# Optimization experiments

Hardware: AMD Instinct MI355X
Metric: run time of the kernel (lower is better)

The kernel has to match this reference:

```python
import jax, jax.numpy as jnp
import numpy as np

N_ATOMS = 10000
N_PAIRS = 100000
H = 64          # hidden_channels
R = 32          # number_of_radial_basis_functions
MAX_Z = 100
CUTOFF = 0.5    # nm (radial_max_distance), min = 0.0


def cosine_cutoff(d):
    # 0.5*(cos(pi*d/rc)+1) for d < rc else 0
    return jnp.where(d < CUTOFF, 0.5 * (jnp.cos(jnp.pi * d / CUTOFF) + 1.0), 0.0)


def expnormal_rbf(d):
    # ExpNormal smearing (TorchMD/TensorNet style), cutoff_lower = 0
    start = float(np.exp(-CUTOFF))
    means = jnp.linspace(start, 1.0, R, dtype=d.dtype)            # [R]
    beta = (2.0 / R * (1.0 - start)) ** -2
    alpha = 5.0 / CUTOFF
    return jnp.exp(-beta * (jnp.exp(-alpha * d)[:, None] - means) ** 2)  # [P,R]


def vector_to_skewtensor(v):
    x, y, z = v[:, 0], v[:, 1], v[:, 2]
    o = jnp.zeros_like(x)
    return jnp.stack([o, -z, y, z, o, -x, -y, x, o], axis=-1).reshape(-1, 3, 3)


def vector_to_symtensor(v):
    t = v[:, :, None] * v[:, None, :]                              # [P,3,3]
    tr3 = (t[:, 0, 0] + t[:, 1, 1] + t[:, 2, 2]) / 3.0
    return t - tr3[:, None, None] * jnp.eye(3, dtype=v.dtype)


def setup_inputs() -> dict:
    key = jax.random.key(0)
    ks = jax.random.split(key, 20)
    atomic_numbers = jax.random.randint(ks[0], (N_ATOMS,), 0, MAX_Z)
    pair_indices = jax.random.randint(ks[1], (2, N_PAIRS), 0, N_ATOMS)
    r_ij = jax.random.normal(ks[2], (N_PAIRS, 3), dtype=jnp.float32) * 0.12  # ~0.2 nm norms
    d_ij = jnp.linalg.norm(r_ij, axis=-1, keepdims=True) + 1e-6
    s = 0.1
    p = {
        'emb':    jax.random.normal(ks[3], (MAX_Z, H)) * s,
        'emb2_w': jax.random.normal(ks[4], (H, 2 * H)) * s,
        'emb2_b': jnp.zeros((H,)),
        'dp1_w':  jax.random.normal(ks[5], (H, R)) * s,
        'dp1_b':  jnp.zeros((H,)),
        'dp2_w':  jax.random.normal(ks[6], (H, R)) * s,
        'dp2_b':  jnp.zeros((H,)),
        'dp3_w':  jax.random.normal(ks[7], (H, R)) * s,
        'dp3_b':  jnp.zeros((H,)),
        'lt0_w':  jax.random.normal(ks[8], (H, H)) * s,
        'lt1_w':  jax.random.normal(ks[9], (H, H)) * s,
        'lt2_w':  jax.random.normal(ks[10], (H, H)) * s,
        'ls1_w':  jax.random.normal(ks[11], (2 * H, H)) * s,
        'ls1_b':  jnp.zeros((2 * H,)),
        'ls2_w':  jax.random.normal(ks[12], (3 * H, 2 * H)) * s,
        'ls2_b':  jnp.zeros((3 * H,)),
        'ln_g':   jnp.ones((H,)),
        'ln_b':   jnp.zeros((H,)),
    }
    return dict(atomic_numbers=atomic_numbers, pair_indices=pair_indices,
                d_ij=d_ij, r_ij=r_ij, **p)


def reference(atomic_numbers, pair_indices, d_ij, r_ij,
              emb, emb2_w, emb2_b, dp1_w, dp1_b, dp2_w, dp2_b, dp3_w, dp3_b,
              lt0_w, lt1_w, lt2_w, ls1_w, ls1_b, ls2_w, ls2_b, ln_g, ln_b):
    n_atoms = atomic_numbers.shape[0]
    src = pair_indices[0]
    # atomic number message Zij: concat(emb[i], emb[j]) -> Linear
    zi = emb[atomic_numbers]                                      # [N,H]
    zij = jnp.concatenate([zi[src], zi[pair_indices[1]]], axis=-1)  # [P,2H]
    Zij = zij @ emb2_w.T + emb2_b                                 # [P,H]
    d = d_ij[:, 0]                                                # [P]
    unit = r_ij / d_ij                                            # [P,3]
    rc = cosine_cutoff(d)                                         # [P]
    rbf = expnormal_rbf(d) * rc[:, None]                          # [P,R]
    C = rc[:, None] * Zij                                         # [P,H]
    f1 = (rbf @ dp1_w.T + dp1_b) * C                              # [P,H]
    f2 = (rbf @ dp2_w.T + dp2_b) * C * 10.0                       # Angstrom scale
    f3 = (rbf @ dp3_w.T + dp3_b) * C * 100.0
    eye = jnp.eye(3, dtype=r_ij.dtype)
    skew = vector_to_skewtensor(unit)                             # [P,3,3]
    sym = vector_to_symtensor(unit)                               # [P,3,3]
    Iij = f1[:, :, None, None] * eye                              # [P,H,3,3]
    Aij = f2[:, :, None, None] * skew[:, None]
    Sij = f3[:, :, None, None] * sym[:, None]
    I = jax.ops.segment_sum(Iij, src, num_segments=n_atoms)       # [N,H,3,3]
    A = jax.ops.segment_sum(Aij, src, num_segments=n_atoms)
    S = jax.ops.segment_sum(Sij, src, num_segments=n_atoms)
    # tensor_norm -> LayerNorm -> scalar MLP
    tn = jnp.sum((I + A + S) ** 2, axis=(-2, -1))                 # [N,H]
    mu = tn.mean(-1, keepdims=True)
    var = tn.var(-1, keepdims=True)
    norm = (tn - mu) / jnp.sqrt(var + 1e-5) * ln_g + ln_b
    norm = jax.nn.silu(norm @ ls1_w.T + ls1_b)
    norm = jax.nn.silu(norm @ ls2_w.T + ls2_b)                    # [N,3H]
    norm = norm.reshape(-1, H, 3)
    I = jnp.einsum('nhij,gh->ngij', I, lt0_w) * norm[:, :, 0][:, :, None, None]
    A = jnp.einsum('nhij,gh->ngij', A, lt1_w) * norm[:, :, 1][:, :, None, None]
    S = jnp.einsum('nhij,gh->ngij', S, lt2_w) * norm[:, :, 2][:, :, None, None]
    return I + A + S
```

## Files before the change

### kernel.cpp

```cpp
#include <hip/hip_runtime.h>
#include <hip/hip_bf16.h>

#define N_ATOMS 10000
#define N_PAIRS 100000
#define HH 64
#define MAXZ 100

typedef _Float16 h2_t __attribute__((ext_vector_type(2)));

constexpr float RBF_START = 0.6065306597126334f;
constexpr float RBF_STEP  = (1.0f - RBF_START) / 31.0f;
constexpr float RBF_BETA  = 1.0f / ((0.0625f * (1.0f - RBF_START)) * (0.0625f * (1.0f - RBF_START)));
constexpr float LOG2E     = 1.4426950408889634f;
constexpr float NEG_ALPHA_L2 = -10.0f * LOG2E;
constexpr float NEG_BETA_L2  = -RBF_BETA * LOG2E;

#define OFF_EMB   0
#define OFF_W2    6400
#define OFF_B2    14592
#define OFF_D1W   14656
#define OFF_D1B   16704
#define OFF_D2W   16768
#define OFF_D2B   18816
#define OFF_D3W   18880
#define OFF_D3B   20928
#define OFF_LT0   20992
#define OFF_LT1   25088
#define OFF_LT2   29184
#define OFF_L1W   33280
#define OFF_L1B   41472
#define OFF_L2W   41600
#define OFF_L2B   66176
#define OFF_LNG   66368
#define OFF_LNB   66432
#define N_PARAMF  66496

#define PH_DP   0
#define PH_L1   3072
#define PH_L2   7168
#define PH_LT   19456
#define PH_N    25600

#define WS_WF     0
#define WS_CNT    266240
#define WS_OFF    307200
#define WS_CUR    348160
#define WS_T1     389120
#define WS_T2     414720
#define WS_PH     440320
#define WS_DPK    542720
#define WS_ZNL    2142720
#define WS_ACCH   2542720

__device__ __forceinline__ float bf2f(unsigned short u) {
    return __uint_as_float(((unsigned int)u) << 16);
}
__device__ __forceinline__ float fexp2(float x) { return __builtin_amdgcn_exp2f(x); }
__device__ __forceinline__ float fcos2pi(float x) { return __builtin_amdgcn_cosf(x); }
__device__ __forceinline__ float fsilu(float x) { return x / (1.0f + fexp2(-LOG2E * x)); }
__device__ __forceinline__ h2_t u2h(unsigned u) { return __builtin_bit_cast(h2_t, u); }
__device__ __forceinline__ unsigned packh2(float a, float b) {
    h2_t v; v.x = (_Float16)a; v.y = (_Float16)b;
    return __builtin_bit_cast(unsigned, v);
}

#if __has_builtin(__builtin_amdgcn_fdot2)
__device__ __forceinline__ float FDOT2(h2_t a, h2_t b, float c) {
    return __builtin_amdgcn_fdot2(a, b, c, false);
}
#else
__device__ __forceinline__ float FDOT2(h2_t a, h2_t b, float c) {
    return c + (float)a.x * (float)b.x + (float)a.y * (float)b.y;
}
#endif
__device__ __forceinline__ float dot16h(const uint4* w, const uint4* x, float acc) {
    uint4 a = *w, b = *x;
    acc = FDOT2(u2h(a.x), u2h(b.x), acc);
    acc = FDOT2(u2h(a.y), u2h(b.y), acc);
    acc = FDOT2(u2h(a.z), u2h(b.z), acc);
    acc = FDOT2(u2h(a.w), u2h(b.w), acc);
    return acc;
}
__device__ __forceinline__ float dot16v(uint4 a, uint4 b, float acc) {
    acc = FDOT2(u2h(a.x), u2h(b.x), acc);
    acc = FDOT2(u2h(a.y), u2h(b.y), acc);
    acc = FDOT2(u2h(a.z), u2h(b.z), acc);
    acc = FDOT2(u2h(a.w), u2h(b.w), acc);
    return acc;
}

__device__ int classify64(const unsigned short* b, int lane) {
    unsigned short x = b[lane];
    int e = (x >> 7) & 0xFF;
    bool implaus = (x != 0) && (e < 96 || e > 133);
    bool zeroeven = ((lane & 1) == 0) && (x == 0);
    unsigned long long mi = __ballot(implaus);
    unsigned long long mz = __ballot(zeroeven);
    if (__popcll(mz) == 32) return 0;
    if (__popcll(mi) >= 8) return 0;
    return 1;
}

struct ConvArgs { const void* src[18]; float* dst; };

__global__ void k_prep(ConvArgs a, const int* __restrict__ pidx, int* __restrict__ cnt) {
    const int sizes[18] = {6400,8192,64,2048,64,2048,64,2048,64,4096,4096,4096,8192,128,24576,192,64,64};
    __shared__ int fl;
    if (threadIdx.x < 64) {
        int f = classify64((const unsigned short*)a.src[0], threadIdx.x);
        if (threadIdx.x == 0) fl = f;
    }
    __syncthreads();
    int t = blockIdx.x * 256 + threadIdx.x;
    if (t < N_PARAMF) {
        int acc = 0, seg = 0, off = t;
        #pragma unroll
        for (int i = 0; i < 18; ++i) {
            if (t >= acc && t < acc + sizes[i]) { seg = i; off = t - acc; }
            acc += sizes[i];
        }
        if (fl == 1) a.dst[t] = bf2f(((const unsigned short*)a.src[seg])[off]);
        else         a.dst[t] = ((const float*)a.src[seg])[off];
    }
    if (t < N_PAIRS) atomicAdd(&cnt[pidx[t]], 1);
}

__global__ void k_tabpack(const float* __restrict__ WF, float* __restrict__ T1,
                          float* __restrict__ T2, unsigned* __restrict__ PH) {
    int z = blockIdx.x;
    int h = threadIdx.x;
    if (h < 64) {
        const float* ez = WF + OFF_EMB + z * HH;
        const float* w2 = WF + OFF_W2 + h * 128;
        float s1 = 0.f, s2 = 0.f;
        #pragma unroll
        for (int k = 0; k < 64; ++k) {
            float e = ez[k];
            s1 += w2[k] * e;
            s2 += w2[64 + k] * e;
        }
        T1[z * HH + h] = s1;
        T2[z * HH + h] = s2;
    }
    int q = blockIdx.x * 256 + threadIdx.x;
    int src;
    if (q < PH_L1) {
        int w = q >> 10, r = q & 1023;
        src = (w == 0 ? OFF_D1W : (w == 1 ? OFF_D2W : OFF_D3W)) + r * 2;
    } else if (q < PH_L2) {
        src = OFF_L1W + (q - PH_L1) * 2;
    } else if (q < PH_LT) {
        src = OFF_L2W + (q - PH_L2) * 2;
    } else {
        src = OFF_LT0 + (q - PH_LT) * 2;
    }
    PH[q] = packh2(WF[src], WF[src + 1]);
}

__global__ void k_scan(const int* __restrict__ cnt, int* __restrict__ offs, int* __restrict__ cur) {
    __shared__ int buf[1024];
    int tid = threadIdx.x;
    int base = tid * 10;
    int c[10]; int s = 0;
    #pragma unroll
    for (int i = 0; i < 10; ++i) {
        int idx = base + i;
        int v = (idx < N_ATOMS) ? cnt[idx] : 0;
        c[i] = v; s += v;
    }
    buf[tid] = s;
    __syncthreads();
    for (int off = 1; off < 1024; off <<= 1) {
        int v = (tid >= off) ? buf[tid - off] : 0;
        __syncthreads();
        buf[tid] += v;
        __syncthreads();
    }
    int run = buf[tid] - s;
    #pragma unroll
    for (int i = 0; i < 10; ++i) {
        int idx = base + i;
        if (idx < N_ATOMS) { offs[idx] = run; cur[idx] = run; run += c[i]; }
    }
    if (tid == 0) offs[N_ATOMS] = N_PAIRS;
}

__global__ void k_fill(const int* __restrict__ pidx, const int* __restrict__ an,
                       const void* __restrict__ dij_v, const void* __restrict__ rij_v,
                       int* __restrict__ cur,
                       float4* __restrict__ dpack, int* __restrict__ znl) {
    __shared__ int fdr[2];
    if (threadIdx.x < 64) {
        int fd = classify64((const unsigned short*)dij_v, threadIdx.x);
        int fr = classify64((const unsigned short*)rij_v, threadIdx.x);
        if (threadIdx.x == 0) { fdr[0] = fd; fdr[1] = fr; }
    }
    __syncthreads();
    int p = blockIdx.x * 256 + threadIdx.x;
    if (p >= N_PAIRS) return;
    int s = pidx[p];
    int dst = pidx[N_PAIRS + p];
    int pos = atomicAdd(&cur[s], 1);
    float d, rx, ry, rz;
    if (fdr[0] == 1) d = bf2f(((const unsigned short*)dij_v)[p]);
    else             d = ((const float*)dij_v)[p];
    if (fdr[1] == 1) {
        const unsigned short* r = (const unsigned short*)rij_v;
        rx = bf2f(r[3*p]); ry = bf2f(r[3*p+1]); rz = bf2f(r[3*p+2]);
    } else {
        const float* r = (const float*)rij_v;
        rx = r[3*p]; ry = r[3*p+1]; rz = r[3*p+2];
    }
    dpack[pos] = make_float4(rx, ry, rz, d);
    znl[pos] = an[dst];
}

__global__ __launch_bounds__(256, 4) void k_pair(
    const int* __restrict__ an,
    const float* __restrict__ WF,
    const int* __restrict__ offs,
    const float4* __restrict__ dpack, const int* __restrict__ znl,
    const float* __restrict__ T1, const float* __restrict__ T2,
    const unsigned* __restrict__ PH,
    unsigned* __restrict__ accH)
{
    __shared__ __align__(16) unsigned rbq[4 * 16];

    const int wave = threadIdx.x >> 6;
    const int h    = threadIdx.x & 63;
    const int n    = blockIdx.x * 4 + wave;

    _Float16* rbfh = (_Float16*)&rbq[wave * 16];
    const uint4* rbp = (const uint4*)&rbq[wave * 16];

    const uint4* g1 = (const uint4*)(PH + PH_DP + 0 * 1024 + h * 16);
    const uint4* g2 = (const uint4*)(PH + PH_DP + 1 * 1024 + h * 16);
    const uint4* g3 = (const uint4*)(PH + PH_DP + 2 * 1024 + h * 16);
    uint4 w1r[4], w2r[4], w3r[4];
    #pragma unroll
    for (int k = 0; k < 4; ++k) {
        w1r[k] = g1[k];
        w2r[k] = g2[k];
        w3r[k] = g3[k];
    }

    const float ed1 = (WF + OFF_D1B)[h];
    const float ed2 = (WF + OFF_D2B)[h];
    const float ed3 = (WF + OFF_D3B)[h];
    const float zA  = (WF + OFF_B2)[h] + T1[an[n] * HH + h];

    float Is=0.f, sx=0.f, sy=0.f, sz=0.f;
    float Sxx=0.f, Syy=0.f, Szz=0.f, Sxy=0.f, Sxz=0.f, Syz=0.f;

    const int pbeg = offs[n], pend = offs[n + 1];

    float4 dp_cur = make_float4(0.f, 0.f, 0.f, 1.f);
    float  t2cur  = 0.f;
    int    zn_n   = 0;
    if (pbeg < pend) {
        dp_cur = dpack[pbeg];
        t2cur  = T2[znl[pbeg] * HH + h];
        if (pbeg + 1 < pend) zn_n = znl[pbeg + 1];
    }

    for (int ii = pbeg; ii < pend; ++ii) {
        const float4 dpv = dp_cur;
        const float  t2v = t2cur;
        if (ii + 1 < pend) {
            dp_cur = dpack[ii + 1];
            t2cur  = T2[zn_n * HH + h];
            if (ii + 2 < pend) zn_n = znl[ii + 2];
        }

        float d = dpv.w;
        float inv = 1.0f / d;
        float ux = dpv.x*inv, uy = dpv.y*inv, uz = dpv.z*inv;
        float rc = (d < 0.5f) ? 0.5f * (fcos2pi(d) + 1.0f) : 0.0f;

        if (h < 32) {
            float en = fexp2(NEG_ALPHA_L2 * d);
            float t = en - (RBF_START + RBF_STEP * (float)h);
            rbfh[h] = (_Float16)(fexp2(NEG_BETA_L2 * t * t) * rc);
        }
        __builtin_amdgcn_wave_barrier();

        float g1a = ed1, g2a = ed2, g3a = ed3;
        #pragma unroll
        for (int k = 0; k < 4; ++k) {
            uint4 rb = rbp[k];
            g1a = dot16v(w1r[k], rb, g1a);
            g2a = dot16v(w2r[k], rb, g2a);
            g3a = dot16v(w3r[k], rb, g3a);
        }

        float zc = zA + t2v;
        float Cc = rc * zc;
        float f1 = g1a * Cc;
        float f2 = g2a * Cc * 10.0f;
        float f3 = g3a * Cc * 100.0f;

        Is += f1;
        sx += f2 * ux;  sy += f2 * uy;  sz += f2 * uz;
        float q = (ux*ux + uy*uy + uz*uz) * (1.0f / 3.0f);
        Sxx += f3 * (ux*ux - q);
        Syy += f3 * (uy*uy - q);
        Szz += f3 * (uz*uz - q);
        Sxy += f3 * (ux*uy);
        Sxz += f3 * (ux*uz);
        Syz += f3 * (uy*uz);
        __builtin_amdgcn_wave_barrier();
    }

    float tn = 3.0f*Is*Is + 2.0f*(sx*sx + sy*sy + sz*sz)
             + Sxx*Sxx + Syy*Syy + Szz*Szz
             + 2.0f*(Sxy*Sxy + Sxz*Sxz + Syz*Syz);
    float s1 = tn, s2 = tn * tn;
    #pragma unroll
    for (int o = 32; o > 0; o >>= 1) {
        s1 += __shfl_xor(s1, o);
        s2 += __shfl_xor(s2, o);
    }
    float mu  = s1 * (1.0f / 64.0f);
    float var = s2 * (1.0f / 64.0f) - mu * mu;
    float nv  = (tn - mu) * rsqrtf(var + 1e-5f) * (WF + OFF_LNG)[h] + (WF + OFF_LNB)[h];

    float vals[11] = {Is, sx, sy, sz, Sxx, Syy, Szz, Sxy, Sxz, Syz, nv};
    #pragma unroll
    for (int c = 0; c < 11; ++c) {
        float pv = __shfl_xor(vals[c], 1);
        if ((h & 1) == 0)
            accH[((n * 11 + c) << 5) + (h >> 1)] = packh2(vals[c], pv);
    }
}

__global__ __launch_bounds__(256, 2) void k_post(
    const float* __restrict__ WF,
    const unsigned* __restrict__ PH,
    const unsigned* __restrict__ accH,
    float* __restrict__ out)
{
    __shared__ __align__(16) unsigned wL2[192 * 68];
    __shared__ __align__(16) unsigned acch[4][12 * 32];
    __shared__ __align__(16) unsigned y1h[4][64];
    __shared__ __align__(16) unsigned y2h[4][96];

    for (int q = threadIdx.x; q < 12288; q += 256) {
        int m = q >> 6, u = q & 63;
        wL2[m * 68 + u] = PH[PH_L2 + q];
    }
    __syncthreads();

    const int wave = threadIdx.x >> 6;
    const int h    = threadIdx.x & 63;
    const int gw   = blockIdx.x * 4 + wave;
    const int GW   = gridDim.x * 4;

    const uint4* l1base = (const uint4*)(PH + PH_L1);
    const uint4* lt0 = (const uint4*)(PH + PH_LT) + h * 8;
    const uint4* lt1 = (const uint4*)(PH + PH_LT + 2048) + h * 8;
    const uint4* lt2 = (const uint4*)(PH + PH_LT + 4096) + h * 8;

    for (int n = gw; n < N_ATOMS; n += GW) {
        if (h < 32) {
            #pragma unroll
            for (int c = 0; c < 11; ++c)
                acch[wave][c * 32 + h] = accH[((n * 11 + c) << 5) + h];
        }
        __builtin_amdgcn_wave_barrier();

        const uint4* nvh = (const uint4*)&acch[wave][10 * 32];

        float ya = (WF + OFF_L1B)[h];
        float yb = (WF + OFF_L1B)[h + 64];
        {
            const uint4* ra = l1base + h * 8;
            const uint4* rb = l1base + (h + 64) * 8;
            #pragma unroll
            for (int k = 0; k < 8; ++k) {
                ya = dot16h(ra + k, nvh + k, ya);
                yb = dot16h(rb + k, nvh + k, yb);
            }
        }
        ya = fsilu(ya); yb = fsilu(yb);
        {
            float pa = __shfl_xor(ya, 1);
            float pb = __shfl_xor(yb, 1);
            if ((h & 1) == 0) {
                y1h[wave][(h >> 1)]      = packh2(ya, pa);
                y1h[wave][32 + (h >> 1)] = packh2(yb, pb);
            }
        }
        __builtin_amdgcn_wave_barrier();

        const uint4* y1p = (const uint4*)&y1h[wave][0];
        float z0 = (WF + OFF_L2B)[h];
        float z1 = (WF + OFF_L2B)[h + 64];
        float z2 = (WF + OFF_L2B)[h + 128];
        {
            const uint4* r0 = (const uint4*)&wL2[(h)       * 68];
            const uint4* r1 = (const uint4*)&wL2[(h + 64)  * 68];
            const uint4* r2 = (const uint4*)&wL2[(h + 128) * 68];
            #pragma unroll
            for (int k = 0; k < 16; ++k) {
                uint4 x = y1p[k];
                uint4 a0 = r0[k], a1 = r1[k], a2 = r2[k];
                z0 = FDOT2(u2h(a0.x), u2h(x.x), z0); z0 = FDOT2(u2h(a0.y), u2h(x.y), z0);
                z0 = FDOT2(u2h(a0.z), u2h(x.z), z0); z0 = FDOT2(u2h(a0.w), u2h(x.w), z0);
                z1 = FDOT2(u2h(a1.x), u2h(x.x), z1); z1 = FDOT2(u2h(a1.y), u2h(x.y), z1);
                z1 = FDOT2(u2h(a1.z), u2h(x.z), z1); z1 = FDOT2(u2h(a1.w), u2h(x.w), z1);
                z2 = FDOT2(u2h(a2.x), u2h(x.x), z2); z2 = FDOT2(u2h(a2.y), u2h(x.y), z2);
                z2 = FDOT2(u2h(a2.z), u2h(x.z), z2); z2 = FDOT2(u2h(a2.w), u2h(x.w), z2);
            }
        }
        z0 = fsilu(z0); z1 = fsilu(z1); z2 = fsilu(z2);
        {
            float p0 = __shfl_xor(z0, 1);
            float p1 = __shfl_xor(z1, 1);
            float p2 = __shfl_xor(z2, 1);
            if ((h & 1) == 0) {
                y2h[wave][(h >> 1)]      = packh2(z0, p0);
                y2h[wave][32 + (h >> 1)] = packh2(z1, p1);
                y2h[wave][64 + (h >> 1)] = packh2(z2, p2);
            }
        }
        __builtin_amdgcn_wave_barrier();

        float n0, n1, n2;
        {
            int i0 = 3 * h;
            unsigned u0 = y2h[wave][i0 >> 1];
            unsigned u1 = y2h[wave][(i0 >> 1) + 1];
            h2_t a = u2h(u0), b = u2h(u1);
            if (i0 & 1) { n0 = (float)a.y; n1 = (float)b.x; n2 = (float)b.y; }
            else        { n0 = (float)a.x; n1 = (float)a.y; n2 = (float)b.x; }
        }

        const uint4* aI  = (const uint4*)&acch[wave][0];
        const uint4* aAx = (const uint4*)&acch[wave][32];
        const uint4* aAy = (const uint4*)&acch[wave][64];
        const uint4* aAz = (const uint4*)&acch[wave][96];
        const uint4* aXX = (const uint4*)&acch[wave][128];
        const uint4* aYY = (const uint4*)&acch[wave][160];
        const uint4* aZZ = (const uint4*)&acch[wave][192];
        const uint4* aXY = (const uint4*)&acch[wave][224];
        const uint4* aXZ = (const uint4*)&acch[wave][256];
        const uint4* aYZ = (const uint4*)&acch[wave][288];

        float P0=0.f, PAx=0.f, PAy=0.f, PAz=0.f;
        float Q0=0.f, Q1=0.f, Q2=0.f, Q3=0.f, Q4=0.f, Q5=0.f;
        #pragma unroll
        for (int k = 0; k < 8; ++k) {
            P0  = dot16h(lt0 + k, aI  + k, P0);
            PAx = dot16h(lt1 + k, aAx + k, PAx);
            PAy = dot16h(lt1 + k, aAy + k, PAy);
            PAz = dot16h(lt1 + k, aAz + k, PAz);
            Q0  = dot16h(lt2 + k, aXX + k, Q0);
            Q1  = dot16h(lt2 + k, aYY + k, Q1);
            Q2  = dot16h(lt2 + k, aZZ + k, Q2);
            Q3  = dot16h(lt2 + k, aXY + k, Q3);
            Q4  = dot16h(lt2 + k, aXZ + k, Q4);
            Q5  = dot16h(lt2 + k, aYZ + k, Q5);
        }
        float Iv = P0 * n0;
        float Ax = PAx * n1, Ay = PAy * n1, Az = PAz * n1;
        float Xx = Q0 * n2, Yy = Q1 * n2, Zz = Q2 * n2;
        float Xy = Q3 * n2, Xz = Q4 * n2, Yz = Q5 * n2;

        float* o = out + (size_t)n * 576 + h * 9;
        o[0] =  Iv + Xx;  o[1] = -Az + Xy;  o[2] =  Ay + Xz;
        o[3] =  Az + Xy;  o[4] =  Iv + Yy;  o[5] = -Ax + Yz;
        o[6] = -Ay + Xz;  o[7] =  Ax + Yz;  o[8] =  Iv + Zz;
        __builtin_amdgcn_wave_barrier();
    }
}

extern "C" void kernel_launch(void* const* d_in, const int* in_sizes, int n_in,
                              void* d_out, int out_size, void* d_ws, size_t ws_size,
                              hipStream_t stream) {
    const int* an   = (const int*)d_in[0];
    const int* pidx = (const int*)d_in[1];

    char* ws = (char*)d_ws;
    float*    WF    = (float*)(ws + WS_WF);
    int*      cnt   = (int*)(ws + WS_CNT);
    int*      offs  = (int*)(ws + WS_OFF);
    int*      cur   = (int*)(ws + WS_CUR);
    float*    T1    = (float*)(ws + WS_T1);
    float*    T2    = (float*)(ws + WS_T2);
    unsigned* PH    = (unsigned*)(ws + WS_PH);
    float4*   dpack = (float4*)(ws + WS_DPK);
    int*      znl   = (int*)(ws + WS_ZNL);
    unsigned* accH  = (unsigned*)(ws + WS_ACCH);
    float*    out   = (float*)d_out;

    hipMemsetAsync(cnt, 0, N_ATOMS * sizeof(int), stream);

    ConvArgs ca;
    for (int i = 0; i < 18; ++i) ca.src[i] = d_in[4 + i];
    ca.dst = WF;
    k_prep<<<(N_PAIRS + 255) / 256, 256, 0, stream>>>(ca, pidx, cnt);
    k_tabpack<<<100, 256, 0, stream>>>(WF, T1, T2, PH);
    k_scan<<<1, 1024, 0, stream>>>(cnt, offs, cur);
    k_fill<<<(N_PAIRS + 255) / 256, 256, 0, stream>>>(pidx, an, d_in[2], d_in[3],
                                                      cur, dpack, znl);
    k_pair<<<2500, 256, 0, stream>>>(an, WF, offs, dpack, znl, T1, T2, PH, accH);
    k_post<<<256, 256, 0, stream>>>(WF, PH, accH, out);
}
```

Baseline: 207.1 us.

## Fuse post-MLP into pair kernel, merge tabpack into prep, shuffle-based scan

Folds the per-atom scalar MLP and linear-transform stage from k_post into k_pair, so the packed accumulators stay in shared memory and no longer round-trip through global workspace. It also merges k_tabpack into k_prep by reading raw inputs directly, and replaces the shared-memory Hillis-Steele scan with wave shuffles. The cost is that every k_pair block now loads a 48KB L2 weight tile into LDS and launch bounds drop to 2 blocks per CU, which lowers occupancy for the pair-gather phase.

```diff
diff --git a/kernel.cpp b/kernel.cpp
--- a/kernel.cpp
+++ b/kernel.cpp
@@ -50,7 +50,6 @@
 #define WS_PH     440320
 #define WS_DPK    542720
 #define WS_ZNL    2142720
-#define WS_ACCH   2542720
 
 __device__ __forceinline__ float bf2f(unsigned short u) {
     return __uint_as_float(((unsigned int)u) << 16);
@@ -101,9 +100,16 @@
     return 1;
 }
 
+__device__ __forceinline__ float ldp(const void* p, int off, int fl) {
+    if (fl == 1) return bf2f(((const unsigned short*)p)[off]);
+    return ((const float*)p)[off];
+}
+
 struct ConvArgs { const void* src[18]; float* dst; };
 
-__global__ void k_prep(ConvArgs a, const int* __restrict__ pidx, int* __restrict__ cnt) {
+__global__ void k_prep(ConvArgs a, const int* __restrict__ pidx, int* __restrict__ cnt,
+                       float* __restrict__ T1, float* __restrict__ T2,
+                       unsigned* __restrict__ PH) {
     const int sizes[18] = {6400,8192,64,2048,64,2048,64,2048,64,4096,4096,4096,8192,128,24576,192,64,64};
     __shared__ int fl;
     if (threadIdx.x < 64) {
@@ -111,55 +117,56 @@
         if (threadIdx.x == 0) fl = f;
     }
     __syncthreads();
-    int t = blockIdx.x * 256 + threadIdx.x;
-    if (t < N_PARAMF) {
-        int acc = 0, seg = 0, off = t;
-        #pragma unroll
-        for (int i = 0; i < 18; ++i) {
-            if (t >= acc && t < acc + sizes[i]) { seg = i; off = t - acc; }
-            acc += sizes[i];
-        }
-        if (fl == 1) a.dst[t] = bf2f(((const unsigned short*)a.src[seg])[off]);
-        else         a.dst[t] = ((const float*)a.src[seg])[off];
-    }
-    if (t < N_PAIRS) atomicAdd(&cnt[pidx[t]], 1);
-}
-
-__global__ void k_tabpack(const float* __restrict__ WF, float* __restrict__ T1,
-                          float* __restrict__ T2, unsigned* __restrict__ PH) {
-    int z = blockIdx.x;
+
+    if (blockIdx.x < 391) {
+        int t = blockIdx.x * 256 + threadIdx.x;
+        if (t < N_PARAMF) {
+            int acc = 0, seg = 0, off = t;
+            #pragma unroll
+            for (int i = 0; i < 18; ++i) {
+                if (t >= acc && t < acc + sizes[i]) { seg = i; off = t - acc; }
+                acc += sizes[i];
+            }
+            a.dst[t] = ldp(a.src[seg], off, fl);
+        }
+        if (t < N_PAIRS) atomicAdd(&cnt[pidx[t]], 1);
+        return;
+    }
+
+    int zb = blockIdx.x - 391;
     int h = threadIdx.x;
     if (h < 64) {
-        const float* ez = WF + OFF_EMB + z * HH;
-        const float* w2 = WF + OFF_W2 + h * 128;
         float s1 = 0.f, s2 = 0.f;
         #pragma unroll
         for (int k = 0; k < 64; ++k) {
-            float e = ez[k];
-            s1 += w2[k] * e;
-            s2 += w2[64 + k] * e;
-        }
-        T1[z * HH + h] = s1;
-        T2[z * HH + h] = s2;
-    }
-    int q = blockIdx.x * 256 + threadIdx.x;
-    int src;
+            float e = ldp(a.src[0], zb * HH + k, fl);
+            s1 += ldp(a.src[1], h * 128 + k, fl) * e;
+            s2 += ldp(a.src[1], h * 128 + 64 + k, fl) * e;
+        }
+        T1[zb * HH + h] = s1;
+        T2[zb * HH + h] = s2;
+    }
+    int q = zb * 256 + threadIdx.x;
+    const void* sp; int off;
     if (q < PH_L1) {
         int w = q >> 10, r = q & 1023;
-        src = (w == 0 ? OFF_D1W : (w == 1 ? OFF_D2W : OFF_D3W)) + r * 2;
+        sp = a.src[3 + 2 * w];
+        off = r * 2;
     } else if (q < PH_L2) {
-        src = OFF_L1W + (q - PH_L1) * 2;
+        sp = a.src[12]; off = (q - PH_L1) * 2;
     } else if (q < PH_LT) {
-        src = OFF_L2W + (q - PH_L2) * 2;
+        sp = a.src[14]; off = (q - PH_L2) * 2;
     } else {
-        src = OFF_LT0 + (q - PH_LT) * 2;
-    }
-    PH[q] = packh2(WF[src], WF[src + 1]);
+        int tt = q - PH_LT;
+        sp = a.src[9 + (tt >> 11)]; off = (tt & 2047) * 2;
+    }
+    PH[q] = packh2(ldp(sp, off, fl), ldp(sp, off + 1, fl));
 }
 
 __global__ void k_scan(const int* __restrict__ cnt, int* __restrict__ offs, int* __restrict__ cur) {
-    __shared__ int buf[1024];
+    __shared__ int wsum[16];
     int tid = threadIdx.x;
+    int lane = tid & 63, wid = tid >> 6;
     int base = tid * 10;
     int c[10]; int s = 0;
     #pragma unroll
@@ -168,15 +175,21 @@
         int v = (idx < N_ATOMS) ? cnt[idx] : 0;
         c[i] = v; s += v;
     }
-    buf[tid] = s;
+    int inc = s;
+    #pragma unroll
+    for (int o = 1; o < 64; o <<= 1) {
+        int v = __shfl_up(inc, o);
+        if (lane >= o) inc += v;
+    }
+    if (lane == 63) wsum[wid] = inc;
     __syncthreads();
-    for (int off = 1; off < 1024; off <<= 1) {
-        int v = (tid >= off) ? buf[tid - off] : 0;
-        __syncthreads();
-        buf[tid] += v;
-        __syncthreads();
-    }
-    int run = buf[tid] - s;
+    int wbase = 0;
+    #pragma unroll
+    for (int w = 0; w < 16; ++w) {
+        int v = wsum[w];
+        if (w < wid) wbase += v;
+    }
+    int run = wbase + (inc - s);
     #pragma unroll
     for (int i = 0; i < 10; ++i) {
         int idx = base + i;
@@ -215,16 +228,28 @@
     znl[pos] = an[dst];
 }
 
-__global__ __launch_bounds__(256, 4) void k_pair(
+__global__ __launch_bounds__(256, 2) void k_pair(
     const int* __restrict__ an,
     const float* __restrict__ WF,
     const int* __restrict__ offs,
     const float4* __restrict__ dpack, const int* __restrict__ znl,
     const float* __restrict__ T1, const float* __restrict__ T2,
     const unsigned* __restrict__ PH,
-    unsigned* __restrict__ accH)
+    float* __restrict__ out)
 {
+    __shared__ __align__(16) unsigned wL2[192 * 68];
     __shared__ __align__(16) unsigned rbq[4 * 16];
+    __shared__ __align__(16) unsigned acch[4][12 * 32];
+    __shared__ __align__(16) unsigned y1h[4][64];
+    __shared__ __align__(16) unsigned y2h[4][96];
+
+    {
+        const uint4* gsrc = (const uint4*)(PH + PH_L2);
+        for (int cch = threadIdx.x; cch < 3072; cch += 256) {
+            uint4 v = gsrc[cch];
+            *((uint4*)&wL2[(cch >> 4) * 68] + (cch & 15)) = v;
+        }
+    }
 
     const int wave = threadIdx.x >> 6;
     const int h    = threadIdx.x & 63;
@@ -324,154 +349,124 @@
     float var = s2 * (1.0f / 64.0f) - mu * mu;
     float nv  = (tn - mu) * rsqrtf(var + 1e-5f) * (WF + OFF_LNG)[h] + (WF + OFF_LNB)[h];
 
+    __syncthreads();
+
     float vals[11] = {Is, sx, sy, sz, Sxx, Syy, Szz, Sxy, Sxz, Syz, nv};
     #pragma unroll
     for (int c = 0; c < 11; ++c) {
         float pv = __shfl_xor(vals[c], 1);
         if ((h & 1) == 0)
-            accH[((n * 11 + c) << 5) + (h >> 1)] = packh2(vals[c], pv);
-    }
-}
-
-__global__ __launch_bounds__(256, 2) void k_post(
-    const float* __restrict__ WF,
-    const unsigned* __restrict__ PH,
-    const unsigned* __restrict__ accH,
-    float* __restrict__ out)
-{
-    __shared__ __align__(16) unsigned wL2[192 * 68];
-    __shared__ __align__(16) unsigned acch[4][12 * 32];
-    __shared__ __align__(16) unsigned y1h[4][64];
-    __shared__ __align__(16) unsigned y2h[4][96];
-
-    for (int q = threadIdx.x; q < 12288; q += 256) {
-        int m = q >> 6, u = q & 63;
-        wL2[m * 68 + u] = PH[PH_L2 + q];
-    }
-    __syncthreads();
-
-    const int wave = threadIdx.x >> 6;
-    const int h    = threadIdx.x & 63;
-    const int gw   = blockIdx.x * 4 + wave;
-    const int GW   = gridDim.x * 4;
-
+            acch[wave][c * 32 + (h >> 1)] = packh2(vals[c], pv);
+    }
+    __builtin_amdgcn_wave_barrier();
+
+    const uint4* nvh = (const uint4*)&acch[wave][10 * 32];
     const uint4* l1base = (const uint4*)(PH + PH_L1);
+
+    float ya = (WF + OFF_L1B)[h];
+    float yb = (WF + OFF_L1B)[h + 64];
+    {
+        const uint4* ra = l1base + h * 8;
+        const uint4* rb = l1base + (h + 64) * 8;
+        #pragma unroll
+        for (int k = 0; k < 8; ++k) {
+            ya = dot16h(ra + k, nvh + k, ya);
+            yb = dot16h(rb + k, nvh + k, yb);
+        }
+    }
+    ya = fsilu(ya); yb = fsilu(yb);
+    {
+        float pa = __shfl_xor(ya, 1);
+        float pb = __shfl_xor(yb, 1);
+        if ((h & 1) == 0) {
+            y1h[wave][(h >> 1)]      = packh2(ya, pa);
+            y1h[wave][32 + (h >> 1)] = packh2(yb, pb);
+        }
+    }
+    __builtin_amdgcn_wave_barrier();
+
+    const uint4* y1p = (const uint4*)&y1h[wave][0];
+    float z0 = (WF + OFF_L2B)[h];
+    float z1 = (WF + OFF_L2B)[h + 64];
+    float z2 = (WF + OFF_L2B)[h + 128];
+    {
+        const uint4* r0 = (const uint4*)&wL2[(h)       * 68];
+        const uint4* r1 = (const uint4*)&wL2[(h + 64)  * 68];
+        const uint4* r2 = (const uint4*)&wL2[(h + 128) * 68];
+        #pragma unroll
+        for (int k = 0; k < 16; ++k) {
+            uint4 x = y1p[k];
+            uint4 a0 = r0[k], a1 = r1[k], a2 = r2[k];
+            z0 = FDOT2(u2h(a0.x), u2h(x.x), z0); z0 = FDOT2(u2h(a0.y), u2h(x.y), z0);
+            z0 = FDOT2(u2h(a0.z), u2h(x.z), z0); z0 = FDOT2(u2h(a0.w), u2h(x.w), z0);
+            z1 = FDOT2(u2h(a1.x), u2h(x.x), z1); z1 = FDOT2(u2h(a1.y), u2h(x.y), z1);
+            z1 = FDOT2(u2h(a1.z), u2h(x.z), z1); z1 = FDOT2(u2h(a1.w), u2h(x.w), z1);
+            z2 = FDOT2(u2h(a2.x), u2h(x.x), z2); z2 = FDOT2(u2h(a2.y), u2h(x.y), z2);
+            z2 = FDOT2(u2h(a2.z), u2h(x.z), z2); z2 = FDOT2(u2h(a2.w), u2h(x.w), z2);
+        }
+    }
+    z0 = fsilu(z0); z1 = fsilu(z1); z2 = fsilu(z2);
+    {
+        float p0 = __shfl_xor(z0, 1);
+        float p1 = __shfl_xor(z1, 1);
+        float p2 = __shfl_xor(z2, 1);
+        if ((h & 1) == 0) {
+            y2h[wave][(h >> 1)]      = packh2(z0, p0);
+            y2h[wave][32 + (h >> 1)] = packh2(z1, p1);
+            y2h[wave][64 + (h >> 1)] = packh2(z2, p2);
+        }
+    }
+    __builtin_amdgcn_wave_barrier();
+
+    float n0, n1, n2;
+    {
+        int i0 = 3 * h;
+        unsigned u0 = y2h[wave][i0 >> 1];
+        unsigned u1 = y2h[wave][(i0 >> 1) + 1];
+        h2_t aa = u2h(u0), bb = u2h(u1);
+        if (i0 & 1) { n0 = (float)aa.y; n1 = (float)bb.x; n2 = (float)bb.y; }
+        else        { n0 = (float)aa.x; n1 = (float)aa.y; n2 = (float)bb.x; }
+    }
+
     const uint4* lt0 = (const uint4*)(PH + PH_LT) + h * 8;
     const uint4* lt1 = (const uint4*)(PH + PH_LT + 2048) + h * 8;
     const uint4* lt2 = (const uint4*)(PH + PH_LT + 4096) + h * 8;
 
-    for (int n = gw; n < N_ATOMS; n += GW) {
-        if (h < 32) {
-            #pragma unroll
-            for (int c = 0; c < 11; ++c)
-                acch[wave][c * 32 + h] = accH[((n * 11 + c) << 5) + h];
-        }
-        __builtin_amdgcn_wave_barrier();
-
-        const uint4* nvh = (const uint4*)&acch[wave][10 * 32];
-
-        float ya = (WF + OFF_L1B)[h];
-        float yb = (WF + OFF_L1B)[h + 64];
-        {
-            const uint4* ra = l1base + h * 8;
-            const uint4* rb = l1base + (h + 64) * 8;
-            #pragma unroll
-            for (int k = 0; k < 8; ++k) {
-                ya = dot16h(ra + k, nvh + k, ya);
-                yb = dot16h(rb + k, nvh + k, yb);
-            }
-        }
-        ya = fsilu(ya); yb = fsilu(yb);
-        {
-            float pa = __shfl_xor(ya, 1);
-            float pb = __shfl_xor(yb, 1);
-            if ((h & 1) == 0) {
-                y1h[wave][(h >> 1)]      = packh2(ya, pa);
-                y1h[wave][32 + (h >> 1)] = packh2(yb, pb);
-            }
-        }
-        __builtin_amdgcn_wave_barrier();
-
-        const uint4* y1p = (const uint4*)&y1h[wave][0];
-        float z0 = (WF + OFF_L2B)[h];
-        float z1 = (WF + OFF_L2B)[h + 64];
-        float z2 = (WF + OFF_L2B)[h + 128];
-        {
-            const uint4* r0 = (const uint4*)&wL2[(h)       * 68];
-            const uint4* r1 = (const uint4*)&wL2[(h + 64)  * 68];
-            const uint4* r2 = (const uint4*)&wL2[(h + 128) * 68];
-            #pragma unroll
-            for (int k = 0; k < 16; ++k) {
-                uint4 x = y1p[k];
-                uint4 a0 = r0[k], a1 = r1[k], a2 = r2[k];
-                z0 = FDOT2(u2h(a0.x), u2h(x.x), z0); z0 = FDOT2(u2h(a0.y), u2h(x.y), z0);
-                z0 = FDOT2(u2h(a0.z), u2h(x.z), z0); z0 = FDOT2(u2h(a0.w), u2h(x.w), z0);
-                z1 = FDOT2(u2h(a1.x), u2h(x.x), z1); z1 = FDOT2(u2h(a1.y), u2h(x.y), z1);
-                z1 = FDOT2(u2h(a1.z), u2h(x.z), z1); z1 = FDOT2(u2h(a1.w), u2h(x.w), z1);
-                z2 = FDOT2(u2h(a2.x), u2h(x.x), z2); z2 = FDOT2(u2h(a2.y), u2h(x.y), z2);
-                z2 = FDOT2(u2h(a2.z), u2h(x.z), z2); z2 = FDOT2(u2h(a2.w), u2h(x.w), z2);
-            }
-        }
-        z0 = fsilu(z0); z1 = fsilu(z1); z2 = fsilu(z2);
-        {
-            float p0 = __shfl_xor(z0, 1);
-            float p1 = __shfl_xor(z1, 1);
-            float p2 = __shfl_xor(z2, 1);
-            if ((h & 1) == 0) {
-                y2h[wave][(h >> 1)]      = packh2(z0, p0);
-                y2h[wave][32 + (h >> 1)] = packh2(z1, p1);
-                y2h[wave][64 + (h >> 1)] = packh2(z2, p2);
-            }
-        }
-        __builtin_amdgcn_wave_barrier();
-
-        float n0, n1, n2;
-        {
-            int i0 = 3 * h;
-            unsigned u0 = y2h[wave][i0 >> 1];
-            unsigned u1 = y2h[wave][(i0 >> 1) + 1];
-            h2_t a = u2h(u0), b = u2h(u1);
-            if (i0 & 1) { n0 = (float)a.y; n1 = (float)b.x; n2 = (float)b.y; }
-            else        { n0 = (float)a.x; n1 = (float)a.y; n2 = (float)b.x; }
-        }
-
-        const uint4* aI  = (const uint4*)&acch[wave][0];
-        const uint4* aAx = (const uint4*)&acch[wave][32];
-        const uint4* aAy = (const uint4*)&acch[wave][64];
-        const uint4* aAz = (const uint4*)&acch[wave][96];
-        const uint4* aXX = (const uint4*)&acch[wave][128];
-        const uint4* aYY = (const uint4*)&acch[wave][160];
-        const uint4* aZZ = (const uint4*)&acch[wave][192];
-        const uint4* aXY = (const uint4*)&acch[wave][224];
-        const uint4* aXZ = (const uint4*)&acch[wave][256];
-        const uint4* aYZ = (const uint4*)&acch[wave][288];
-
-        float P0=0.f, PAx=0.f, PAy=0.f, PAz=0.f;
-        float Q0=0.f, Q1=0.f, Q2=0.f, Q3=0.f, Q4=0.f, Q5=0.f;
-        #pragma unroll
-        for (int k = 0; k < 8; ++k) {
-            P0  = dot16h(lt0 + k, aI  + k, P0);
-            PAx = dot16h(lt1 + k, aAx + k, PAx);
-            PAy = dot16h(lt1 + k, aAy + k, PAy);
-            PAz = dot16h(lt1 + k, aAz + k, PAz);
-            Q0  = dot16h(lt2 + k, aXX + k, Q0);
-            Q1  = dot16h(lt2 + k, aYY + k, Q1);
-            Q2  = dot16h(lt2 + k, aZZ + k, Q2);
-            Q3  = dot16h(lt2 + k, aXY + k, Q3);
-            Q4  = dot16h(lt2 + k, aXZ + k, Q4);
-            Q5  = dot16h(lt2 + k, aYZ + k, Q5);
-        }
-        float Iv = P0 * n0;
-        float Ax = PAx * n1, Ay = PAy * n1, Az = PAz * n1;
-        float Xx = Q0 * n2, Yy = Q1 * n2, Zz = Q2 * n2;
-        float Xy = Q3 * n2, Xz = Q4 * n2, Yz = Q5 * n2;
-
-        float* o = out + (size_t)n * 576 + h * 9;
-        o[0] =  Iv + Xx;  o[1] = -Az + Xy;  o[2] =  Ay + Xz;
-        o[3] =  Az + Xy;  o[4] =  Iv + Yy;  o[5] = -Ax + Yz;
-        o[6] = -Ay + Xz;  o[7] =  Ax + Yz;  o[8] =  Iv + Zz;
-        __builtin_amdgcn_wave_barrier();
-    }
+    const uint4* aI  = (const uint4*)&acch[wave][0];
+    const uint4* aAx = (const uint4*)&acch[wave][32];
+    const uint4* aAy = (const uint4*)&acch[wave][64];
+    const uint4* aAz = (const uint4*)&acch[wave][96];
+    const uint4* aXX = (const uint4*)&acch[wave][128];
+    const uint4* aYY = (const uint4*)&acch[wave][160];
+    const uint4* aZZ = (const uint4*)&acch[wave][192];
+    const uint4* aXY = (const uint4*)&acch[wave][224];
+    const uint4* aXZ = (const uint4*)&acch[wave][256];
+    const uint4* aYZ = (const uint4*)&acch[wave][288];
+
+    float P0=0.f, PAx=0.f, PAy=0.f, PAz=0.f;
+    float Q0=0.f, Q1=0.f, Q2=0.f, Q3=0.f, Q4=0.f, Q5=0.f;
+    #pragma unroll
+    for (int k = 0; k < 8; ++k) {
+        P0  = dot16h(lt0 + k, aI  + k, P0);
+        PAx = dot16h(lt1 + k, aAx + k, PAx);
+        PAy = dot16h(lt1 + k, aAy + k, PAy);
+        PAz = dot16h(lt1 + k, aAz + k, PAz);
+        Q0  = dot16h(lt2 + k, aXX + k, Q0);
+        Q1  = dot16h(lt2 + k, aYY + k, Q1);
+        Q2  = dot16h(lt2 + k, aZZ + k, Q2);
+        Q3  = dot16h(lt2 + k, aXY + k, Q3);
+        Q4  = dot16h(lt2 + k, aXZ + k, Q4);
+        Q5  = dot16h(lt2 + k, aYZ + k, Q5);
+    }
+    float Iv = P0 * n0;
+    float Ax = PAx * n1, Ay = PAy * n1, Az = PAz * n1;
+    float Xx = Q0 * n2, Yy = Q1 * n2, Zz = Q2 * n2;
+    float Xy = Q3 * n2, Xz = Q4 * n2, Yz = Q5 * n2;
+
+    float* o = out + (size_t)n * 576 + h * 9;
+    o[0] =  Iv + Xx;  o[1] = -Az + Xy;  o[2] =  Ay + Xz;
+    o[3] =  Az + Xy;  o[4] =  Iv + Yy;  o[5] = -Ax + Yz;
+    o[6] = -Ay + Xz;  o[7] =  Ax + Yz;  o[8] =  Iv + Zz;
 }
 
 extern "C" void kernel_launch(void* const* d_in, const int* in_sizes, int n_in,
@@ -490,7 +485,6 @@
     unsigned* PH    = (unsigned*)(ws + WS_PH);
     float4*   dpack = (float4*)(ws + WS_DPK);
     int*      znl   = (int*)(ws + WS_ZNL);
-    unsigned* accH  = (unsigned*)(ws + WS_ACCH);
     float*    out   = (float*)d_out;
 
     hipMemsetAsync(cnt, 0, N_ATOMS * sizeof(int), stream);
@@ -498,11 +492,9 @@
     ConvArgs ca;
     for (int i = 0; i < 18; ++i) ca.src[i] = d_in[4 + i];
     ca.dst = WF;
-    k_prep<<<(N_PAIRS + 255) / 256, 256, 0, stream>>>(ca, pidx, cnt);
-    k_tabpack<<<100, 256, 0, stream>>>(WF, T1, T2, PH);
+    k_prep<<<491, 256, 0, stream>>>(ca, pidx, cnt, T1, T2, PH);
     k_scan<<<1, 1024, 0, stream>>>(cnt, offs, cur);
     k_fill<<<(N_PAIRS + 255) / 256, 256, 0, stream>>>(pidx, an, d_in[2], d_in[3],
                                                       cur, dpack, znl);
-    k_pair<<<2500, 256, 0, stream>>>(an, WF, offs, dpack, znl, T1, T2, PH, accH);
-    k_post<<<256, 256, 0, stream>>>(WF, PH, accH, out);
-}
+    k_pair<<<2500, 256, 0, stream>>>(an, WF, offs, dpack, znl, T1, T2, PH, out);
+}
```

After: 255.0 us. +23.1%, slower.
